# Optimization experiments

Hardware: AMD Instinct MI355X
Metric: run time of the kernel (lower is better)

## Reference

```python
import jax, jax.numpy as jnp
import numpy as np

N_NODES, N_EDGES = 50000, 25000
MAX_ARITY, MAX_DEG = 6, 8
NFEAT, NHID, NEMB, NHEADS = 128, 64, 128, 4
BATCH = 4096
ALPHA = 0.2
NEG = -1e9


def _attn_layer(hn_in, he_in, edge_list, node_list, Wn, We, a1, a2, concat):
    # hn_in [N,fin_n], he_in [E,fin_e]; edge_list [E,A] 1-based (0=pad); node_list [N,D] 1-based (0=pad)
    hn = hn_in @ Wn                      # [N,d]
    he = he_in @ We                      # [E,d]
    # --- stage 1: node -> edge attention ---
    emask = edge_list > 0                # [E,A]
    eidx = jnp.where(emask, edge_list - 1, 0)
    nd = hn[eidx]                        # [E,A,d]
    he_b = jnp.broadcast_to(he[:, None, :], nd.shape)
    s1 = jax.nn.leaky_relu(jnp.concatenate([he_b, nd], -1) @ a1, ALPHA)  # [E,A]
    att1 = jax.nn.softmax(jnp.where(emask, s1, NEG), axis=-1)
    edge_out = jnp.einsum('ea,ead->ed', att1, nd)  # [E,d]
    # --- stage 2: edge -> node attention ---
    nmask = node_list > 0                # [N,D]
    nidx = jnp.where(nmask, node_list - 1, 0)
    ed = edge_out[nidx]                  # [N,D,d]
    hn_b = jnp.broadcast_to(hn[:, None, :], ed.shape)
    s2 = jax.nn.leaky_relu(jnp.concatenate([hn_b, ed], -1) @ a2, ALPHA)  # [N,D]
    att2 = jax.nn.softmax(jnp.where(nmask, s2, NEG), axis=-1)
    node_out = jnp.einsum('nd,nde->ne', att2, ed)  # [N,d]
    if concat:
        node_out, edge_out = jax.nn.elu(node_out), jax.nn.elu(edge_out)
    return node_out, edge_out


def _forward(batch_inputs, edge_list, node_list, node_embs, edge_embs,
             Wn, We, a1, a2, Wn_o, We_o, a1_o, a2_o):
    # multi-head layers (vmap over head-stacked params)
    heads = jax.vmap(_attn_layer, in_axes=(None, None, None, None, 0, 0, 0, 0, None))
    hn, he = heads(node_embs, edge_embs, edge_list, node_list, Wn, We, a1, a2, True)
    H, N, d = hn.shape
    out_n = jnp.transpose(hn, (1, 0, 2)).reshape(N, H * d)          # concat heads
    out_e = jnp.transpose(he, (1, 0, 2)).reshape(he.shape[1], H * d)
    # dropout is identity in eval mode
    out_n, out_e = _attn_layer(out_n, out_e, edge_list, node_list, Wn_o, We_o, a1_o, a2_o, False)
    out_n, out_e = jax.nn.elu(out_n), jax.nn.elu(out_e)
    # --- build batch_outputs ---
    B, A1 = batch_inputs.shape
    nemb = out_e.shape[1]
    row0 = out_e[batch_inputs[:, 0] - 1]                            # [B,nemb] (col0 always >0)
    nids = batch_inputs[:, 1:] - 1
    nids = jnp.where(nids < 0, nids + out_n.shape[0], nids)         # torch-style negative wrap
    gathered = out_n[nids]                                          # [B,A1-1,nemb]
    last_nz = jnp.max(jnp.where(batch_inputs != 0, jnp.arange(A1)[None, :], -1), axis=1)  # right-1
    fill = (jnp.arange(1, A1)[None, :] <= last_nz[:, None])[:, :, None]
    rest = jnp.where(fill, gathered, jnp.ones((), gathered.dtype))
    return jnp.concatenate([row0[:, None, :], rest], axis=1)        # [B,A1,nemb]


def setup_inputs() -> dict:
    key = jax.random.key(0)
    ks = jax.random.split(key, 12)
    f32 = jnp.float32
    node_embs = jax.random.normal(ks[0], (N_NODES, NFEAT), f32) * 0.02
    edge_embs = jax.random.normal(ks[1], (N_EDGES, NFEAT), f32) * 0.02
    # ragged incidence with 0-padding (1-based ids)
    el = jax.random.randint(ks[2], (N_EDGES, MAX_ARITY), 1, N_NODES + 1)
    earity = jax.random.randint(ks[3], (N_EDGES, 1), 2, MAX_ARITY + 1)
    edge_list = jnp.where(jnp.arange(MAX_ARITY)[None, :] < earity, el, 0)
    nl = jax.random.randint(ks[4], (N_NODES, MAX_DEG), 1, N_EDGES + 1)
    ndeg = jax.random.randint(ks[5], (N_NODES, 1), 1, MAX_DEG + 1)
    node_list = jnp.where(jnp.arange(MAX_DEG)[None, :] < ndeg, nl, 0)
    # batch: col0 = edge id, cols 1.. = node ids, right-padded with 0
    bi_e = jax.random.randint(ks[6], (BATCH, 1), 1, N_EDGES + 1)
    bi_n = jax.random.randint(ks[7], (BATCH, MAX_ARITY), 1, N_NODES + 1)
    barity = jax.random.randint(ks[8], (BATCH, 1), 2, MAX_ARITY + 1)
    bi_n = jnp.where(jnp.arange(MAX_ARITY)[None, :] < barity, bi_n, 0)
    batch_inputs = jnp.concatenate([bi_e, bi_n], axis=1)
    def glorot(k, shape):
        lim = np.sqrt(6.0 / (shape[-2] + shape[-1]))
        return jax.random.uniform(k, shape, f32, -lim, lim)
    return {
        'batch_inputs': batch_inputs, 'edge_list': edge_list, 'node_list': node_list,
        'node_embs': node_embs, 'edge_embs': edge_embs,
        'Wn': glorot(ks[9], (NHEADS, NFEAT, NHID)),
        'We': glorot(ks[10], (NHEADS, NFEAT, NHID)),
        'a1': jax.random.normal(ks[11], (NHEADS, 2 * NHID), f32) * 0.1,
        'a2': jax.random.normal(jax.random.fold_in(key, 20), (NHEADS, 2 * NHID), f32) * 0.1,
        'Wn_o': glorot(jax.random.fold_in(key, 21), (NHID * NHEADS, NEMB)),
        'We_o': glorot(jax.random.fold_in(key, 22), (NHID * NHEADS, NEMB)),
        'a1_o': jax.random.normal(jax.random.fold_in(key, 23), (2 * NEMB,), f32) * 0.1,
        'a2_o': jax.random.normal(jax.random.fold_in(key, 24), (2 * NEMB,), f32) * 0.1,
    }


def reference(batch_inputs, edge_list, node_list, node_embs, edge_embs,
              Wn, We, a1, a2, Wn_o, We_o, a1_o, a2_o):
    return _forward(batch_inputs, edge_list, node_list, node_embs, edge_embs,
                    Wn, We, a1, a2, Wn_o, We_o, a1_o, a2_o)
```

## Files before the change

### kernel.cpp

```cpp
#include <hip/hip_runtime.h>
#include <math.h>

#define N_NODES 50000
#define N_EDGES 25000
#define MAX_ARITY 6
#define MAX_DEG 8
#define NFEAT 128
#define NHID 64
#define NEMB 128
#define NHEADS 4
#define BATCH 4096

#define MT_N 3128

typedef __bf16 bf16x8 __attribute__((ext_vector_type(8)));
typedef __bf16 bf16x4 __attribute__((ext_vector_type(4)));
typedef float f32x4 __attribute__((ext_vector_type(4)));
typedef float f32x2 __attribute__((ext_vector_type(2)));

__device__ __forceinline__ float wave_sum(float v) {
#pragma unroll
    for (int off = 1; off < 64; off <<= 1) v += __shfl_xor(v, off);
    return v;
}
__device__ __forceinline__ float group32_sum(float v) {
#pragma unroll
    for (int off = 1; off < 32; off <<= 1) v += __shfl_xor(v, off);
    return v;
}
__device__ __forceinline__ float group16_sum(float v) {
#pragma unroll
    for (int off = 1; off < 16; off <<= 1) v += __shfl_xor(v, off);
    return v;
}
__device__ __forceinline__ float group8_sum(float v) {
#pragma unroll
    for (int off = 1; off < 8; off <<= 1) v += __shfl_xor(v, off);
    return v;
}
__device__ __forceinline__ float lrelu(float x) { return x >= 0.f ? x : 0.2f * x; }
__device__ __forceinline__ float eluf(float x) { return x > 0.f ? x : expm1f(x); }

__device__ __forceinline__ int2 pack_fp8x8(const float* v) {
    int w0 = __builtin_amdgcn_cvt_pk_fp8_f32(v[0], v[1], 0, 0);
    w0 = __builtin_amdgcn_cvt_pk_fp8_f32(v[2], v[3], w0, 1);
    int w1 = __builtin_amdgcn_cvt_pk_fp8_f32(v[4], v[5], 0, 0);
    w1 = __builtin_amdgcn_cvt_pk_fp8_f32(v[6], v[7], w1, 1);
    int2 o;
    o.x = w0;
    o.y = w1;
    return o;
}
__device__ __forceinline__ void unpack_fp8x8(int2 w, float* v) {
    f32x2 a = __builtin_amdgcn_cvt_pk_f32_fp8(w.x, false);
    f32x2 b = __builtin_amdgcn_cvt_pk_f32_fp8(w.x, true);
    f32x2 c = __builtin_amdgcn_cvt_pk_f32_fp8(w.y, false);
    f32x2 d = __builtin_amdgcn_cvt_pk_f32_fp8(w.y, true);
    v[0] = a[0]; v[1] = a[1]; v[2] = b[0]; v[3] = b[1];
    v[4] = c[0]; v[5] = c[1]; v[6] = d[0]; v[7] = d[1];
}
__device__ __forceinline__ unsigned char fp8_of(float x) {
    return (unsigned char)(__builtin_amdgcn_cvt_pk_fp8_f32(x, x, 0, 0) & 0xff);
}

#define PREP_BCONV1_BLKS 16
#define PREP_BCONV2_BLKS 16
#define PREP_WVEC1_BLKS 2
#define PREP_WVEC2_BLKS 1
#define PREP_C1_BLKS 6250
#define PREP_TOTAL_BLKS (PREP_BCONV1_BLKS + PREP_BCONV2_BLKS + \
                         PREP_WVEC1_BLKS + PREP_WVEC2_BLKS + PREP_C1_BLKS)

__global__ __launch_bounds__(256) void prep_kernel(
    const float* __restrict__ edge_embs, const float* __restrict__ Wn,
    const float* __restrict__ We, const float* __restrict__ a1, const float* __restrict__ Wn_o,
    const float* __restrict__ We_o, const float* __restrict__ a1_o, __bf16* __restrict__ B1n,
    __bf16* __restrict__ B2n, float* __restrict__ wc1, float* __restrict__ wc2,
    float* __restrict__ c1) {
    int blk = blockIdx.x;
    if (blk < PREP_BCONV1_BLKS) {
        int t = blk * 256 + threadIdx.x;
        int lane = t & 63;
        int nt = (t >> 6) & 15;
        int kt = t >> 10;
        int k0 = kt * 32 + (lane >> 4) * 8;
        int h = nt >> 2;
        int nl = (nt & 3) * 16 + (lane & 15);
        bf16x8 o;
#pragma unroll
        for (int j = 0; j < 8; ++j) o[j] = (__bf16)Wn[(h * NFEAT + k0 + j) * NHID + nl];
        reinterpret_cast<bf16x8*>(B1n)[t] = o;
        return;
    }
    blk -= PREP_BCONV1_BLKS;
    if (blk < PREP_BCONV2_BLKS) {
        int t = blk * 256 + threadIdx.x;
        int lane = t & 63;
        int nt = (t >> 6) & 7;
        int kt = t >> 9;
        int k0 = kt * 32 + (lane >> 4) * 8;
        int n = nt * 16 + (lane & 15);
        bf16x8 o;
#pragma unroll
        for (int j = 0; j < 8; ++j) o[j] = (__bf16)Wn_o[(size_t)(k0 + j) * 128 + n];
        reinterpret_cast<bf16x8*>(B2n)[t] = o;
        return;
    }
    blk -= PREP_BCONV2_BLKS;
    if (blk < PREP_WVEC1_BLKS) {
        int t = blk * 256 + threadIdx.x;
        int h = t >> 7, k = t & 127;
        float s = 0.f;
        for (int j = 0; j < 64; ++j) s += We[(h * NFEAT + k) * NHID + j] * a1[h * 128 + j];
        wc1[t] = s;
        return;
    }
    blk -= PREP_WVEC1_BLKS;
    if (blk < PREP_WVEC2_BLKS) {
        int t = threadIdx.x;
        float s = 0.f;
        for (int j = 0; j < 128; ++j) s += We_o[(size_t)t * 128 + j] * a1_o[j];
        wc2[t] = s;
        return;
    }
    blk -= PREP_WVEC2_BLKS;
    {
        int r = blk * 4 + (threadIdx.x >> 6);
        int lane = threadIdx.x & 63;
        if (r >= N_EDGES) return;
        float x0 = edge_embs[(size_t)r * 128 + lane];
        float x1 = edge_embs[(size_t)r * 128 + 64 + lane];
#pragma unroll
        for (int h = 0; h < 4; ++h) {
            float s = wave_sum(x0 * wc1[h * 128 + lane] + x1 * wc1[h * 128 + 64 + lane]);
            if (lane == 0) c1[r * 4 + h] = s;
        }
    }
}

__global__ __launch_bounds__(256) void mgemm1_kernel(
    const float* __restrict__ Af32, const __bf16* __restrict__ B,
    unsigned char* __restrict__ C, const float* __restrict__ a1v,
    const float* __restrict__ a2v, float* __restrict__ d1, float* __restrict__ g1v) {
    const int w = threadIdx.x >> 6, l = threadIdx.x & 63;
    const int mtb = blockIdx.y * 8 + w * 2;
    const int nbf = blockIdx.x * 4;
    const int lr = l & 15, lk = (l >> 4) * 8;
    f32x4 acc[2][4];
#pragma unroll
    for (int i = 0; i < 2; ++i)
#pragma unroll
        for (int j = 0; j < 4; ++j) acc[i][j] = (f32x4){0.f, 0.f, 0.f, 0.f};
    const bf16x8* Bp = reinterpret_cast<const bf16x8*>(B) + l;
#pragma unroll
    for (int kt = 0; kt < 4; ++kt) {
        bf16x8 a[2];
#pragma unroll
        for (int mi = 0; mi < 2; ++mi) {
            int row = (mtb + mi) * 16 + lr;
            int ks = kt * 32 + lk;
            float v[8];
            if (row < N_NODES) {
                float4 p0 = *reinterpret_cast<const float4*>(Af32 + (size_t)row * 128 + ks);
                float4 p1 = *reinterpret_cast<const float4*>(Af32 + (size_t)row * 128 + ks + 4);
                v[0] = p0.x; v[1] = p0.y; v[2] = p0.z; v[3] = p0.w;
                v[4] = p1.x; v[5] = p1.y; v[6] = p1.z; v[7] = p1.w;
            } else {
#pragma unroll
                for (int j = 0; j < 8; ++j) v[j] = 0.f;
            }
#pragma unroll
            for (int j = 0; j < 8; ++j) a[mi][j] = (__bf16)v[j];
        }
#pragma unroll
        for (int nj = 0; nj < 4; ++nj) {
            bf16x8 b = Bp[((size_t)kt * 16 + nbf + nj) * 64];
#pragma unroll
            for (int mi = 0; mi < 2; ++mi)
                acc[mi][nj] = __builtin_amdgcn_mfma_f32_16x16x32_bf16(a[mi], b, acc[mi][nj], 0, 0, 0);
        }
    }
    const int rq = (l >> 4) * 4;
    const int cl = l & 15;
    const int h = nbf >> 2;
    float va[4], vb[4];
#pragma unroll
    for (int nj = 0; nj < 4; ++nj) {
        int col = ((nbf + nj) & 3) * 16 + cl;
        va[nj] = a1v[h * 128 + 64 + col];
        vb[nj] = a2v[h * 128 + col];
    }
#pragma unroll
    for (int mi = 0; mi < 2; ++mi) {
#pragma unroll
        for (int q = 0; q < 4; ++q) {
            int m = (mtb + mi) * 16 + rq + q;
            float pA = 0.f, pB = 0.f;
#pragma unroll
            for (int nj = 0; nj < 4; ++nj) {
                pA += acc[mi][nj][q] * va[nj];
                pB += acc[mi][nj][q] * vb[nj];
            }
            if (m < N_NODES) {
#pragma unroll
                for (int nj = 0; nj < 4; ++nj)
                    C[(size_t)m * 256 + (nbf + nj) * 16 + cl] = fp8_of(acc[mi][nj][q]);
            }
            pA = group16_sum(pA);
            pB = group16_sum(pB);
            if (cl == 0 && m < N_NODES) {
                d1[m * 4 + h] = pA;
                g1v[m * 4 + h] = pB;
            }
        }
    }
}

__global__ __launch_bounds__(256) void mgemm2_kernel(
    const __bf16* __restrict__ A, const __bf16* __restrict__ B, __bf16* __restrict__ C,
    const float* __restrict__ a1o, const float* __restrict__ a2o, float* __restrict__ d2,
    float* __restrict__ g2v) {
    const int w = threadIdx.x >> 6, l = threadIdx.x & 63;
    const int mtb = blockIdx.y * 4 + w;
    f32x4 acc[8];
#pragma unroll
    for (int j = 0; j < 8; ++j) acc[j] = (f32x4){0.f, 0.f, 0.f, 0.f};
    const bf16x8* Ap = reinterpret_cast<const bf16x8*>(A) + (size_t)mtb * 8 * 64 + l;
    const bf16x8* Bp = reinterpret_cast<const bf16x8*>(B) + l;
#pragma unroll
    for (int kt = 0; kt < 8; ++kt) {
        bf16x8 a = Ap[(size_t)kt * 64];
#pragma unroll
        for (int nj = 0; nj < 8; ++nj) {
            bf16x8 b = Bp[((size_t)kt * 8 + nj) * 64];
            acc[nj] = __builtin_amdgcn_mfma_f32_16x16x32_bf16(a, b, acc[nj], 0, 0, 0);
        }
    }
    const int rq = (l >> 4) * 4;
    const int cl = l & 15;
    float va[8], vb[8];
#pragma unroll
    for (int nj = 0; nj < 8; ++nj) {
        va[nj] = a1o[128 + nj * 16 + cl];
        vb[nj] = a2o[nj * 16 + cl];
    }
#pragma unroll
    for (int q = 0; q < 4; ++q) {
        int m = mtb * 16 + rq + q;
        float pA = 0.f, pB = 0.f;
#pragma unroll
        for (int nj = 0; nj < 8; ++nj) {
            pA += acc[nj][q] * va[nj];
            pB += acc[nj][q] * vb[nj];
        }
        if (m < N_NODES) {
#pragma unroll
            for (int nj = 0; nj < 8; ++nj)
                C[(size_t)m * 128 + nj * 16 + cl] = (__bf16)acc[nj][q];
        }
        pA = group16_sum(pA);
        pB = group16_sum(pB);
        if (cl == 0 && m < N_NODES) {
            d2[m] = pA;
            g2v[m] = pB;
        }
    }
}

__global__ __launch_bounds__(256) void attn64e_kernel(
    const int* __restrict__ nbr, const unsigned char* __restrict__ feat,
    const float* __restrict__ sdot, const float* __restrict__ ndot,
    const float* __restrict__ a2v, const float* __restrict__ wc2,
    unsigned char* __restrict__ eo1, float* __restrict__ f1, float* __restrict__ c2, int rows) {
    const int lane = threadIdx.x & 63;
    const int half = lane >> 5, lp = lane & 31;
    const int r = (blockIdx.x * 4 + (threadIdx.x >> 6)) * 2 + half;
    if (r >= rows) return;
    const int h = lp >> 3;
    int id[MAX_ARITY];
    bool val[MAX_ARITY];
#pragma unroll
    for (int a = 0; a < MAX_ARITY; ++a) {
        int v = nbr[r * MAX_ARITY + a];
        val[a] = v > 0;
        id[a] = val[a] ? (v - 1) : 0;
    }
    int2 f8[MAX_ARITY];
    float nd[MAX_ARITY];
#pragma unroll
    for (int a = 0; a < MAX_ARITY; ++a) {
        f8[a] = *reinterpret_cast<const int2*>(feat + (size_t)id[a] * 256 + lp * 8);
        nd[a] = ndot[(size_t)id[a] * 4 + h];
    }
    const float c = sdot[r * 4 + h];
    float wgt[MAX_ARITY];
    float smax = -1e30f;
#pragma unroll
    for (int a = 0; a < MAX_ARITY; ++a) {
        float s = val[a] ? lrelu(c + nd[a]) : -3e30f;
        wgt[a] = s;
        if (val[a]) smax = fmaxf(smax, s);
    }
    float denom = 0.f;
#pragma unroll
    for (int a = 0; a < MAX_ARITY; ++a) {
        float ex = val[a] ? expf(wgt[a] - smax) : 0.f;
        wgt[a] = ex;
        denom += ex;
    }
    float inv = 1.f / denom;
    float acc[8] = {0.f, 0.f, 0.f, 0.f, 0.f, 0.f, 0.f, 0.f};
#pragma unroll
    for (int a = 0; a < MAX_ARITY; ++a) {
        float fv[8];
        unpack_fp8x8(f8[a], fv);
#pragma unroll
        for (int j = 0; j < 8; ++j) acc[j] = fmaf(wgt[a], fv[j], acc[j]);
    }
#pragma unroll
    for (int j = 0; j < 8; ++j) acc[j] *= inv;
    *reinterpret_cast<int2*>(eo1 + (size_t)r * 256 + lp * 8) = pack_fp8x8(acc);
    float p = 0.f;
#pragma unroll
    for (int j = 0; j < 8; ++j) p += acc[j] * a2v[h * 128 + 64 + (lp & 7) * 8 + j];
    p = group8_sum(p);
    if ((lp & 7) == 0) f1[r * 4 + h] = p;
    float p2 = 0.f;
#pragma unroll
    for (int j = 0; j < 8; ++j) p2 += eluf(acc[j]) * wc2[lp * 8 + j];
    p2 = group32_sum(p2);
    if (lp == 0) c2[r] = p2;
}

__global__ __launch_bounds__(256) void attn64n_kernel(const int* __restrict__ nbr,
                                                      const unsigned char* __restrict__ feat,
                                                      const float* __restrict__ sdot,
                                                      const float* __restrict__ ndot,
                                                      __bf16* __restrict__ Afrag, int rows,
                                                      int rowsPad) {
    const int lane = threadIdx.x & 63;
    const int half = lane >> 5, lp = lane & 31;
    const int r = (blockIdx.x * 4 + (threadIdx.x >> 6)) * 2 + half;
    if (r >= rowsPad) return;
    const int rr = r & 15, mt = r >> 4;
    const int kt = lp >> 2, g = lp & 3;
    __bf16* dptr = Afrag + ((((size_t)mt * 8 + kt) * 64 + g * 16 + rr) << 3);
    if (r >= rows) {
        bf16x8 z;
#pragma unroll
        for (int j = 0; j < 8; ++j) z[j] = (__bf16)0.f;
        *reinterpret_cast<bf16x8*>(dptr) = z;
        return;
    }
    const int h = lp >> 3;
    int id[MAX_DEG];
    bool val[MAX_DEG];
#pragma unroll
    for (int a = 0; a < MAX_DEG; ++a) {
        int v = nbr[r * MAX_DEG + a];
        val[a] = v > 0;
        id[a] = val[a] ? (v - 1) : 0;
    }
    int2 f8[MAX_DEG];
    float nd[MAX_DEG];
#pragma unroll
    for (int a = 0; a < MAX_DEG; ++a) {
        f8[a] = *reinterpret_cast<const int2*>(feat + (size_t)id[a] * 256 + lp * 8);
        nd[a] = ndot[(size_t)id[a] * 4 + h];
    }
    const float c = sdot[r * 4 + h];
    float wgt[MAX_DEG];
    float smax = -1e30f;
#pragma unroll
    for (int a = 0; a < MAX_DEG; ++a) {
        float s = val[a] ? lrelu(c + nd[a]) : -3e30f;
        wgt[a] = s;
        if (val[a]) smax = fmaxf(smax, s);
    }
    float denom = 0.f;
#pragma unroll
    for (int a = 0; a < MAX_DEG; ++a) {
        float ex = val[a] ? expf(wgt[a] - smax) : 0.f;
        wgt[a] = ex;
        denom += ex;
    }
    float inv = 1.f / denom;
    float acc[8] = {0.f, 0.f, 0.f, 0.f, 0.f, 0.f, 0.f, 0.f};
#pragma unroll
    for (int a = 0; a < MAX_DEG; ++a) {
        float fv[8];
        unpack_fp8x8(f8[a], fv);
#pragma unroll
        for (int j = 0; j < 8; ++j) acc[j] = fmaf(wgt[a], fv[j], acc[j]);
    }
    bf16x8 o;
#pragma unroll
    for (int j = 0; j < 8; ++j) o[j] = (__bf16)eluf(acc[j] * inv);
    *reinterpret_cast<bf16x8*>(dptr) = o;
}

__global__ __launch_bounds__(256) void attn128e_kernel(
    const int* __restrict__ nbr, const __bf16* __restrict__ feat,
    const float* __restrict__ sdot, const float* __restrict__ ndot,
    const float* __restrict__ fvec, __bf16* __restrict__ outF, float* __restrict__ outDot,
    int rows) {
    const int lane = threadIdx.x & 63;
    const int qt = lane >> 4, lq = lane & 15;
    const int r = (blockIdx.x * 4 + (threadIdx.x >> 6)) * 4 + qt;
    if (r >= rows) return;
    int id[MAX_ARITY];
    bool val[MAX_ARITY];
#pragma unroll
    for (int a = 0; a < MAX_ARITY; ++a) {
        int v = nbr[r * MAX_ARITY + a];
        val[a] = v > 0;
        id[a] = val[a] ? (v - 1) : 0;
    }
    bf16x8 f8[MAX_ARITY];
    float nd[MAX_ARITY];
#pragma unroll
    for (int a = 0; a < MAX_ARITY; ++a) {
        f8[a] = *reinterpret_cast<const bf16x8*>(feat + (size_t)id[a] * 128 + lq * 8);
        nd[a] = ndot[id[a]];
    }
    const float c = sdot[r];
    float wgt[MAX_ARITY];
    float smax = -1e30f;
#pragma unroll
    for (int a = 0; a < MAX_ARITY; ++a) {
        float s = val[a] ? lrelu(c + nd[a]) : -3e30f;
        wgt[a] = s;
        if (val[a]) smax = fmaxf(smax, s);
    }
    float denom = 0.f;
#pragma unroll
    for (int a = 0; a < MAX_ARITY; ++a) {
        float ex = val[a] ? expf(wgt[a] - smax) : 0.f;
        wgt[a] = ex;
        denom += ex;
    }
    float inv = 1.f / denom;
    float acc[8] = {0.f, 0.f, 0.f, 0.f, 0.f, 0.f, 0.f, 0.f};
#pragma unroll
    for (int a = 0; a < MAX_ARITY; ++a)
#pragma unroll
        for (int j = 0; j < 8; ++j) acc[j] = fmaf(wgt[a], (float)f8[a][j], acc[j]);
    bf16x8 o;
#pragma unroll
    for (int j = 0; j < 8; ++j) {
        acc[j] *= inv;
        o[j] = (__bf16)acc[j];
    }
    *reinterpret_cast<bf16x8*>(outF + (size_t)r * 128 + lq * 8) = o;
    float p = 0.f;
#pragma unroll
    for (int j = 0; j < 8; ++j) p += acc[j] * fvec[128 + lq * 8 + j];
    p = group16_sum(p);
    if (lq == 0) outDot[r] = p;
}

__global__ __launch_bounds__(256) void batch2_kernel(
    const int* __restrict__ bi, const int* __restrict__ node_list,
    const __bf16* __restrict__ eo2, const float* __restrict__ g2v,
    const float* __restrict__ f2, float* __restrict__ out) {
    const int lane = threadIdx.x & 63;
    const int half = lane >> 5, lp = lane & 31;
    const int gw = (blockIdx.x * 4 + (threadIdx.x >> 6)) * 2 + half;
    if (gw >= BATCH * 7) return;
    const int b = gw / 7, s = gw % 7;
    int last_nz = -1;
#pragma unroll
    for (int j = 0; j < 7; ++j)
        if (bi[b * 7 + j] != 0) last_nz = j;
    float4 v;
    if (s == 0) {
        int e = bi[b * 7] - 1;
        bf16x4 t = *reinterpret_cast<const bf16x4*>(eo2 + (size_t)e * 128 + lp * 4);
        v = make_float4(eluf((float)t[0]), eluf((float)t[1]), eluf((float)t[2]),
                        eluf((float)t[3]));
    } else if (s <= last_nz) {
        int nid = bi[b * 7 + s] - 1;
        int id[MAX_DEG];
        bool val[MAX_DEG];
#pragma unroll
        for (int a = 0; a < MAX_DEG; ++a) {
            int e = node_list[nid * MAX_DEG + a];
            val[a] = e > 0;
            id[a] = val[a] ? (e - 1) : 0;
        }
        bf16x4 f8[MAX_DEG];
        float nd[MAX_DEG];
#pragma unroll
        for (int a = 0; a < MAX_DEG; ++a) {
            f8[a] = *reinterpret_cast<const bf16x4*>(eo2 + (size_t)id[a] * 128 + lp * 4);
            nd[a] = f2[id[a]];
        }
        const float c = g2v[nid];
        float wgt[MAX_DEG];
        float smax = -1e30f;
#pragma unroll
        for (int a = 0; a < MAX_DEG; ++a) {
            float sc = val[a] ? lrelu(c + nd[a]) : -3e30f;
            wgt[a] = sc;
            if (val[a]) smax = fmaxf(smax, sc);
        }
        float denom = 0.f;
#pragma unroll
        for (int a = 0; a < MAX_DEG; ++a) {
            float ex = val[a] ? expf(wgt[a] - smax) : 0.f;
            wgt[a] = ex;
            denom += ex;
        }
        float inv = 1.f / denom;
        float acc[4] = {0.f, 0.f, 0.f, 0.f};
#pragma unroll
        for (int a = 0; a < MAX_DEG; ++a)
#pragma unroll
            for (int j = 0; j < 4; ++j) acc[j] = fmaf(wgt[a], (float)f8[a][j], acc[j]);
        v = make_float4(eluf(acc[0] * inv), eluf(acc[1] * inv), eluf(acc[2] * inv),
                        eluf(acc[3] * inv));
    } else {
        v = make_float4(1.f, 1.f, 1.f, 1.f);
    }
    *reinterpret_cast<float4*>(out + (size_t)b * 896 + s * 128 + lp * 4) = v;
}

extern "C" void kernel_launch(void* const* d_in, const int* in_sizes, int n_in,
                              void* d_out, int out_size, void* d_ws, size_t ws_size,
                              hipStream_t stream) {
    const int* batch_inputs = (const int*)d_in[0];
    const int* edge_list = (const int*)d_in[1];
    const int* node_list = (const int*)d_in[2];
    const float* node_embs = (const float*)d_in[3];
    const float* edge_embs = (const float*)d_in[4];
    const float* Wn = (const float*)d_in[5];
    const float* We = (const float*)d_in[6];
    const float* a1 = (const float*)d_in[7];
    const float* a2 = (const float*)d_in[8];
    const float* Wn_o = (const float*)d_in[9];
    const float* We_o = (const float*)d_in[10];
    const float* a1_o = (const float*)d_in[11];
    const float* a2_o = (const float*)d_in[12];
    float* out = (float*)d_out;
    char* ws = (char*)d_ws;

    __bf16* B1n = (__bf16*)(ws);
    __bf16* B2n = (__bf16*)(ws + 65536);
    float* wc1 = (float*)(ws + 131072);
    float* wc2 = (float*)(ws + 133120);
    float* c1 = (float*)(ws + 134144);
    float* d1 = (float*)(ws + 534144);
    float* g1v = (float*)(ws + 1334144);
    float* f1 = (float*)(ws + 2134144);
    float* c2 = (float*)(ws + 2534144);
    float* d2 = (float*)(ws + 2634144);
    float* g2v = (float*)(ws + 2834144);
    float* f2 = (float*)(ws + 3034144);
    unsigned char* hn1 = (unsigned char*)(ws + 3134144);
    __bf16* A2n = (__bf16*)(ws + 15934144);
    __bf16* hn2 = (__bf16*)(ws + 41558720);
    unsigned char* eo1 = (unsigned char*)(ws + 54358720);
    __bf16* eo2 = (__bf16*)(ws + 60758720);

    prep_kernel<<<PREP_TOTAL_BLKS, 256, 0, stream>>>(edge_embs, Wn, We, a1, Wn_o, We_o, a1_o,
                                                     B1n, B2n, wc1, wc2, c1);

    {
        dim3 g(4, MT_N / 8);
        mgemm1_kernel<<<g, 256, 0, stream>>>(node_embs, B1n, hn1, a1, a2, d1, g1v);
    }
    attn64e_kernel<<<(N_EDGES / 2 + 3) / 4, 256, 0, stream>>>(edge_list, hn1, c1, d1, a2, wc2,
                                                              eo1, f1, c2, N_EDGES);
    attn64n_kernel<<<(MT_N * 16 / 2 + 3) / 4, 256, 0, stream>>>(node_list, eo1, g1v, f1, A2n,
                                                                N_NODES, MT_N * 16);
    {
        dim3 g(1, MT_N / 4);
        mgemm2_kernel<<<g, 256, 0, stream>>>(A2n, B2n, hn2, a1_o, a2_o, d2, g2v);
    }
    attn128e_kernel<<<(N_EDGES / 4 + 3) / 4, 256, 0, stream>>>(edge_list, hn2, c2, d2, a2_o,
                                                               eo2, f2, N_EDGES);
    batch2_kernel<<<(BATCH * 7 / 2 + 3) / 4, 256, 0, stream>>>(batch_inputs, node_list, eo2,
                                                               g2v, f2, out);
}
```

Baseline: 209.1 us.

## Merge edge-score projection into first GEMM launch and widen GEMM tile

```diff
diff --git a/kernel.cpp b/kernel.cpp
--- a/kernel.cpp
+++ b/kernel.cpp
@@ -67,16 +67,13 @@
 #define PREP_BCONV2_BLKS 16
 #define PREP_WVEC1_BLKS 2
 #define PREP_WVEC2_BLKS 1
-#define PREP_C1_BLKS 6250
-#define PREP_TOTAL_BLKS (PREP_BCONV1_BLKS + PREP_BCONV2_BLKS + \
-                         PREP_WVEC1_BLKS + PREP_WVEC2_BLKS + PREP_C1_BLKS)
+#define PREP_TOTAL_BLKS (PREP_BCONV1_BLKS + PREP_BCONV2_BLKS + PREP_WVEC1_BLKS + PREP_WVEC2_BLKS)
 
 __global__ __launch_bounds__(256) void prep_kernel(
-    const float* __restrict__ edge_embs, const float* __restrict__ Wn,
-    const float* __restrict__ We, const float* __restrict__ a1, const float* __restrict__ Wn_o,
-    const float* __restrict__ We_o, const float* __restrict__ a1_o, __bf16* __restrict__ B1n,
-    __bf16* __restrict__ B2n, float* __restrict__ wc1, float* __restrict__ wc2,
-    float* __restrict__ c1) {
+    const float* __restrict__ Wn, const float* __restrict__ We, const float* __restrict__ a1,
+    const float* __restrict__ Wn_o, const float* __restrict__ We_o,
+    const float* __restrict__ a1_o, __bf16* __restrict__ B1n, __bf16* __restrict__ B2n,
+    float* __restrict__ wc1, float* __restrict__ wc2) {
     int blk = blockIdx.x;
     if (blk < PREP_BCONV1_BLKS) {
         int t = blk * 256 + threadIdx.x;
@@ -115,17 +112,25 @@
         wc1[t] = s;
         return;
     }
-    blk -= PREP_WVEC1_BLKS;
-    if (blk < PREP_WVEC2_BLKS) {
+    {
         int t = threadIdx.x;
         float s = 0.f;
         for (int j = 0; j < 128; ++j) s += We_o[(size_t)t * 128 + j] * a1_o[j];
         wc2[t] = s;
-        return;
-    }
-    blk -= PREP_WVEC2_BLKS;
-    {
-        int r = blk * 4 + (threadIdx.x >> 6);
+    }
+}
+
+#define MEGA1_GEMM_BLKS (MT_N / 4)
+#define MEGA1_C1_BLKS 6250
+#define MEGA1_TOTAL_BLKS (MEGA1_GEMM_BLKS + MEGA1_C1_BLKS)
+
+__global__ __launch_bounds__(256) void mega1_kernel(
+    const float* __restrict__ Af32, const float* __restrict__ edge_embs,
+    const __bf16* __restrict__ B, unsigned char* __restrict__ C, const float* __restrict__ a1v,
+    const float* __restrict__ a2v, const float* __restrict__ wc1, float* __restrict__ d1,
+    float* __restrict__ g1v, float* __restrict__ c1) {
+    if (blockIdx.x >= MEGA1_GEMM_BLKS) {
+        int r = (blockIdx.x - MEGA1_GEMM_BLKS) * 4 + (threadIdx.x >> 6);
         int lane = threadIdx.x & 63;
         if (r >= N_EDGES) return;
         float x0 = edge_embs[(size_t)r * 128 + lane];
@@ -135,29 +140,20 @@
             float s = wave_sum(x0 * wc1[h * 128 + lane] + x1 * wc1[h * 128 + 64 + lane]);
             if (lane == 0) c1[r * 4 + h] = s;
         }
-    }
-}
-
-__global__ __launch_bounds__(256) void mgemm1_kernel(
-    const float* __restrict__ Af32, const __bf16* __restrict__ B,
-    unsigned char* __restrict__ C, const float* __restrict__ a1v,
-    const float* __restrict__ a2v, float* __restrict__ d1, float* __restrict__ g1v) {
+        return;
+    }
     const int w = threadIdx.x >> 6, l = threadIdx.x & 63;
-    const int mtb = blockIdx.y * 8 + w * 2;
-    const int nbf = blockIdx.x * 4;
+    const int mtb = blockIdx.x * 4 + w;
     const int lr = l & 15, lk = (l >> 4) * 8;
-    f32x4 acc[2][4];
-#pragma unroll
-    for (int i = 0; i < 2; ++i)
-#pragma unroll
-        for (int j = 0; j < 4; ++j) acc[i][j] = (f32x4){0.f, 0.f, 0.f, 0.f};
+    f32x4 acc[16];
+#pragma unroll
+    for (int j = 0; j < 16; ++j) acc[j] = (f32x4){0.f, 0.f, 0.f, 0.f};
     const bf16x8* Bp = reinterpret_cast<const bf16x8*>(B) + l;
+    const int row = mtb * 16 + lr;
 #pragma unroll
     for (int kt = 0; kt < 4; ++kt) {
-        bf16x8 a[2];
-#pragma unroll
-        for (int mi = 0; mi < 2; ++mi) {
-            int row = (mtb + mi) * 16 + lr;
+        bf16x8 a;
+        {
             int ks = kt * 32 + lk;
             float v[8];
             if (row < N_NODES) {
@@ -170,41 +166,32 @@
                 for (int j = 0; j < 8; ++j) v[j] = 0.f;
             }
 #pragma unroll
-            for (int j = 0; j < 8; ++j) a[mi][j] = (__bf16)v[j];
-        }
-#pragma unroll
-        for (int nj = 0; nj < 4; ++nj) {
-            bf16x8 b = Bp[((size_t)kt * 16 + nbf + nj) * 64];
-#pragma unroll
-            for (int mi = 0; mi < 2; ++mi)
-                acc[mi][nj] = __builtin_amdgcn_mfma_f32_16x16x32_bf16(a[mi], b, acc[mi][nj], 0, 0, 0);
+            for (int j = 0; j < 8; ++j) a[j] = (__bf16)v[j];
+        }
+#pragma unroll
+        for (int nj = 0; nj < 16; ++nj) {
+            bf16x8 b = Bp[((size_t)kt * 16 + nj) * 64];
+            acc[nj] = __builtin_amdgcn_mfma_f32_16x16x32_bf16(a, b, acc[nj], 0, 0, 0);
         }
     }
     const int rq = (l >> 4) * 4;
     const int cl = l & 15;
-    const int h = nbf >> 2;
-    float va[4], vb[4];
-#pragma unroll
-    for (int nj = 0; nj < 4; ++nj) {
-        int col = ((nbf + nj) & 3) * 16 + cl;
-        va[nj] = a1v[h * 128 + 64 + col];
-        vb[nj] = a2v[h * 128 + col];
-    }
-#pragma unroll
-    for (int mi = 0; mi < 2; ++mi) {
-#pragma unroll
-        for (int q = 0; q < 4; ++q) {
-            int m = (mtb + mi) * 16 + rq + q;
+#pragma unroll
+    for (int q = 0; q < 4; ++q) {
+        int m = mtb * 16 + rq + q;
+        if (m < N_NODES) {
+#pragma unroll
+            for (int nj = 0; nj < 16; ++nj)
+                C[(size_t)m * 256 + nj * 16 + cl] = fp8_of(acc[nj][q]);
+        }
+#pragma unroll
+        for (int h = 0; h < 4; ++h) {
             float pA = 0.f, pB = 0.f;
 #pragma unroll
-            for (int nj = 0; nj < 4; ++nj) {
-                pA += acc[mi][nj][q] * va[nj];
-                pB += acc[mi][nj][q] * vb[nj];
-            }
-            if (m < N_NODES) {
-#pragma unroll
-                for (int nj = 0; nj < 4; ++nj)
-                    C[(size_t)m * 256 + (nbf + nj) * 16 + cl] = fp8_of(acc[mi][nj][q]);
+            for (int j = 0; j < 4; ++j) {
+                int col = j * 16 + cl;
+                pA += acc[h * 4 + j][q] * a1v[h * 128 + 64 + col];
+                pB += acc[h * 4 + j][q] * a2v[h * 128 + col];
             }
             pA = group16_sum(pA);
             pB = group16_sum(pB);
@@ -212,57 +199,6 @@
                 d1[m * 4 + h] = pA;
                 g1v[m * 4 + h] = pB;
             }
-        }
-    }
-}
-
-__global__ __launch_bounds__(256) void mgemm2_kernel(
-    const __bf16* __restrict__ A, const __bf16* __restrict__ B, __bf16* __restrict__ C,
-    const float* __restrict__ a1o, const float* __restrict__ a2o, float* __restrict__ d2,
-    float* __restrict__ g2v) {
-    const int w = threadIdx.x >> 6, l = threadIdx.x & 63;
-    const int mtb = blockIdx.y * 4 + w;
-    f32x4 acc[8];
-#pragma unroll
-    for (int j = 0; j < 8; ++j) acc[j] = (f32x4){0.f, 0.f, 0.f, 0.f};
-    const bf16x8* Ap = reinterpret_cast<const bf16x8*>(A) + (size_t)mtb * 8 * 64 + l;
-    const bf16x8* Bp = reinterpret_cast<const bf16x8*>(B) + l;
-#pragma unroll
-    for (int kt = 0; kt < 8; ++kt) {
-        bf16x8 a = Ap[(size_t)kt * 64];
-#pragma unroll
-        for (int nj = 0; nj < 8; ++nj) {
-            bf16x8 b = Bp[((size_t)kt * 8 + nj) * 64];
-            acc[nj] = __builtin_amdgcn_mfma_f32_16x16x32_bf16(a, b, acc[nj], 0, 0, 0);
-        }
-    }
-    const int rq = (l >> 4) * 4;
-    const int cl = l & 15;
-    float va[8], vb[8];
-#pragma unroll
-    for (int nj = 0; nj < 8; ++nj) {
-        va[nj] = a1o[128 + nj * 16 + cl];
-        vb[nj] = a2o[nj * 16 + cl];
-    }
-#pragma unroll
-    for (int q = 0; q < 4; ++q) {
-        int m = mtb * 16 + rq + q;
-        float pA = 0.f, pB = 0.f;
-#pragma unroll
-        for (int nj = 0; nj < 8; ++nj) {
-            pA += acc[nj][q] * va[nj];
-            pB += acc[nj][q] * vb[nj];
-        }
-        if (m < N_NODES) {
-#pragma unroll
-            for (int nj = 0; nj < 8; ++nj)
-                C[(size_t)m * 128 + nj * 16 + cl] = (__bf16)acc[nj][q];
-        }
-        pA = group16_sum(pA);
-        pB = group16_sum(pB);
-        if (cl == 0 && m < N_NODES) {
-            d2[m] = pA;
-            g2v[m] = pB;
         }
     }
 }
@@ -397,6 +333,57 @@
 #pragma unroll
     for (int j = 0; j < 8; ++j) o[j] = (__bf16)eluf(acc[j] * inv);
     *reinterpret_cast<bf16x8*>(dptr) = o;
+}
+
+__global__ __launch_bounds__(256) void mgemm2_kernel(
+    const __bf16* __restrict__ A, const __bf16* __restrict__ B, __bf16* __restrict__ C,
+    const float* __restrict__ a1o, const float* __restrict__ a2o, float* __restrict__ d2,
+    float* __restrict__ g2v) {
+    const int w = threadIdx.x >> 6, l = threadIdx.x & 63;
+    const int mtb = blockIdx.y * 4 + w;
+    f32x4 acc[8];
+#pragma unroll
+    for (int j = 0; j < 8; ++j) acc[j] = (f32x4){0.f, 0.f, 0.f, 0.f};
+    const bf16x8* Ap = reinterpret_cast<const bf16x8*>(A) + (size_t)mtb * 8 * 64 + l;
+    const bf16x8* Bp = reinterpret_cast<const bf16x8*>(B) + l;
+#pragma unroll
+    for (int kt = 0; kt < 8; ++kt) {
+        bf16x8 a = Ap[(size_t)kt * 64];
+#pragma unroll
+        for (int nj = 0; nj < 8; ++nj) {
+            bf16x8 b = Bp[((size_t)kt * 8 + nj) * 64];
+            acc[nj] = __builtin_amdgcn_mfma_f32_16x16x32_bf16(a, b, acc[nj], 0, 0, 0);
+        }
+    }
+    const int rq = (l >> 4) * 4;
+    const int cl = l & 15;
+    float va[8], vb[8];
+#pragma unroll
+    for (int nj = 0; nj < 8; ++nj) {
+        va[nj] = a1o[128 + nj * 16 + cl];
+        vb[nj] = a2o[nj * 16 + cl];
+    }
+#pragma unroll
+    for (int q = 0; q < 4; ++q) {
+        int m = mtb * 16 + rq + q;
+        float pA = 0.f, pB = 0.f;
+#pragma unroll
+        for (int nj = 0; nj < 8; ++nj) {
+            pA += acc[nj][q] * va[nj];
+            pB += acc[nj][q] * vb[nj];
+        }
+        if (m < N_NODES) {
+#pragma unroll
+            for (int nj = 0; nj < 8; ++nj)
+                C[(size_t)m * 128 + nj * 16 + cl] = (__bf16)acc[nj][q];
+        }
+        pA = group16_sum(pA);
+        pB = group16_sum(pB);
+        if (cl == 0 && m < N_NODES) {
+            d2[m] = pA;
+            g2v[m] = pB;
+        }
+    }
 }
 
 __global__ __launch_bounds__(256) void attn128e_kernel(
@@ -562,13 +549,10 @@
     unsigned char* eo1 = (unsigned char*)(ws + 54358720);
     __bf16* eo2 = (__bf16*)(ws + 60758720);
 
-    prep_kernel<<<PREP_TOTAL_BLKS, 256, 0, stream>>>(edge_embs, Wn, We, a1, Wn_o, We_o, a1_o,
-                                                     B1n, B2n, wc1, wc2, c1);
-
-    {
-        dim3 g(4, MT_N / 8);
-        mgemm1_kernel<<<g, 256, 0, stream>>>(node_embs, B1n, hn1, a1, a2, d1, g1v);
-    }
+    prep_kernel<<<PREP_TOTAL_BLKS, 256, 0, stream>>>(Wn, We, a1, Wn_o, We_o, a1_o, B1n, B2n,
+                                                     wc1, wc2);
+    mega1_kernel<<<MEGA1_TOTAL_BLKS, 256, 0, stream>>>(node_embs, edge_embs, B1n, hn1, a1, a2,
+                                                       wc1, d1, g1v, c1);
     attn64e_kernel<<<(N_EDGES / 2 + 3) / 4, 256, 0, stream>>>(edge_list, hn1, c1, d1, a2, wc2,
                                                               eo1, f1, c2, N_EDGES);
     attn64n_kernel<<<(MT_N * 16 / 2 + 3) / 4, 256, 0, stream>>>(node_list, eo1, g1v, f1, A2n,
```

New measurement: 220.5 us. 1.05x slower.
